# Kernel tuning notes

Hardware: AMD Instinct MI355X
Metric: run time of the kernel (lower is better)

## Reference

```python
import jax, jax.numpy as jnp
import numpy as np

N = 50000        # nodes
E = 1_600_000    # edges (avg degree 32)
G = 512          # graphs in batch
H = 128          # hidden
C_IN = 3
C_MID = 64
C_OUT = 2
EPS = 1e-5


def setup_inputs() -> dict:
    key = jax.random.key(0)
    ks = jax.random.split(key, 16)
    inp = {
        "x": jax.random.normal(ks[0], (N, C_IN), dtype=jnp.float32),
        "edge_index": jax.random.randint(ks[1], (2, E), 0, N, dtype=jnp.int64),
        "batch": jnp.sort(jax.random.randint(ks[2], (N,), 0, G, dtype=jnp.int64)),
        # GCNConv weights (PyG: out = norm_agg(x @ W) + b)
        "W1": jax.random.normal(ks[3], (C_IN, H), dtype=jnp.float32) / np.sqrt(C_IN),
        "b1": jnp.zeros((H,), jnp.float32),
        "W2": jax.random.normal(ks[4], (H, H), dtype=jnp.float32) / np.sqrt(H),
        "b2": jnp.zeros((H,), jnp.float32),
        "W3": jax.random.normal(ks[5], (H, H), dtype=jnp.float32) / np.sqrt(H),
        "b3": jnp.zeros((H,), jnp.float32),
        # BatchNorm affine params (input_bn, bn1, bn2, bn3)
        "bn0_g": jnp.ones((C_IN,), jnp.float32), "bn0_b": jnp.zeros((C_IN,), jnp.float32),
        "bn1_g": jnp.ones((H,), jnp.float32), "bn1_b": jnp.zeros((H,), jnp.float32),
        "bn2_g": jnp.ones((H,), jnp.float32), "bn2_b": jnp.zeros((H,), jnp.float32),
        "bn3_g": jnp.ones((H,), jnp.float32), "bn3_b": jnp.zeros((H,), jnp.float32),
        # classifier MLP
        "Wc1": jax.random.normal(ks[6], (H, C_MID), dtype=jnp.float32) / np.sqrt(H),
        "bc1": jnp.zeros((C_MID,), jnp.float32),
        "Wc2": jax.random.normal(ks[7], (C_MID, C_OUT), dtype=jnp.float32) / np.sqrt(C_MID),
        "bc2": jnp.zeros((C_OUT,), jnp.float32),
    }
    return inp


def _batchnorm(h, g, b):
    # training-mode BN over node dim (biased variance, as torch uses for normalization)
    m = h.mean(axis=0)
    v = jnp.mean((h - m) ** 2, axis=0)
    return (h - m) * jax.lax.rsqrt(v + EPS) * g + b


def _gcn_conv(h, W, b, src, dst, deg_inv_sqrt, deg_inv):
    # PyG GCNConv: symmetric normalization with self-loops.
    hw = h @ W                                        # [N, out]
    coef = deg_inv_sqrt[src] * deg_inv_sqrt[dst]      # [E]
    msg = hw[src] * coef[:, None]                     # [E, out]
    agg = jax.ops.segment_sum(msg, dst, num_segments=N)
    agg = agg + hw * deg_inv[:, None]                 # self-loop term (norm = 1/deg)
    return agg + b


def reference(x, edge_index, batch, W1, b1, W2, b2, W3, b3,
              bn0_g, bn0_b, bn1_g, bn1_b, bn2_g, bn2_b, bn3_g, bn3_b,
              Wc1, bc1, Wc2, bc2):
    src, dst = edge_index[0], edge_index[1]
    # degree with self-loops (in-degree at dst + 1)
    deg = jax.ops.segment_sum(jnp.ones((E,), jnp.float32), dst, num_segments=N) + 1.0
    deg_inv_sqrt = jax.lax.rsqrt(deg)
    deg_inv = 1.0 / deg

    h = _batchnorm(x, bn0_g, bn0_b)
    h = _batchnorm(jax.nn.relu(_gcn_conv(h, W1, b1, src, dst, deg_inv_sqrt, deg_inv)), bn1_g, bn1_b)
    h = _batchnorm(jax.nn.relu(_gcn_conv(h, W2, b2, src, dst, deg_inv_sqrt, deg_inv)), bn2_g, bn2_b)
    h = _batchnorm(jax.nn.relu(_gcn_conv(h, W3, b3, src, dst, deg_inv_sqrt, deg_inv)), bn3_g, bn3_b)

    # global mean pool over graphs
    sums = jax.ops.segment_sum(h, batch, num_segments=G)            # [G, H]
    cnts = jax.ops.segment_sum(jnp.ones((N,), jnp.float32), batch, num_segments=G)
    pooled = sums / jnp.maximum(cnts, 1.0)[:, None]

    # classifier (dropout = identity in eval)
    z = jax.nn.relu(pooled @ Wc1 + bc1)
    return z @ Wc2 + bc2
```

## Files before the change

kernel.cpp:

```cpp
#include <hip/hip_runtime.h>

#define NEPS 1e-5f

__device__ inline unsigned int bfpack(float a, float b) {
  unsigned int ua = __float_as_uint(a), ub = __float_as_uint(b);
  ua += 0x7fff + ((ua >> 16) & 1);
  ub += 0x7fff + ((ub >> 16) & 1);
  return (ua >> 16) | (ub & 0xffff0000u);
}
__device__ inline float bflo(unsigned int u) { return __uint_as_float(u << 16); }
__device__ inline float bfhi(unsigned int u) { return __uint_as_float(u & 0xffff0000u); }

__device__ inline int blockScan256(int v, int t, int* tmp) {
  int lane = t & 63, w = t >> 6;
  #pragma unroll
  for (int off = 1; off < 64; off <<= 1) {
    int u = __shfl_up(v, off);
    if (lane >= off) v += u;
  }
  if (lane == 63) tmp[w] = v;
  __syncthreads();
  int add = 0;
  for (int k = 0; k < w; k++) add += tmp[k];
  return v + add;
}

__global__ __launch_bounds__(256) void k_hist(const int* __restrict__ ei,
                                              int* __restrict__ gh_pad, int E_) {
  __shared__ int h[256];
  int t = threadIdx.x;
  h[t] = 0;
  __syncthreads();
  int i = blockIdx.x * 256 + t;
  int stride = gridDim.x * 256;
  for (int e = i; e < E_; e += stride) atomicAdd(&h[ei[E_ + e] >> 8], 1);
  __syncthreads();
  int c = h[t];
  if (c) atomicAdd(&gh_pad[t * 16], c);
}

__global__ __launch_bounds__(256) void k_scan2(const int* __restrict__ gh_pad,
                                               int* __restrict__ b_base,
                                               int* __restrict__ cur_pad, int E_) {
  __shared__ int tmp[4];
  int t = threadIdx.x;
  int c = gh_pad[t * 16];
  int incl = blockScan256(c, t, tmp);
  int excl = incl - c;
  b_base[t] = excl;
  cur_pad[t * 16] = excl;
  if (t == 255) b_base[256] = incl;
}

__global__ __launch_bounds__(256) void k_part(const int* __restrict__ ei,
                                              int* __restrict__ cur_pad,
                                              unsigned int* __restrict__ kp, int E_) {
  __shared__ int lh[256], lbase[256];
  int t = threadIdx.x;
  int start = blockIdx.x * 8192;
  int end = min(start + 8192, E_);
  lh[t] = 0;
  __syncthreads();
  for (int e = start + t; e < end; e += 256) atomicAdd(&lh[ei[E_ + e] >> 8], 1);
  __syncthreads();
  int c = lh[t];
  if (c) lbase[t] = atomicAdd(&cur_pad[t * 16], c);
  __syncthreads();
  lh[t] = 0;
  __syncthreads();
  for (int e = start + t; e < end; e += 256) {
    int d = ei[E_ + e], s = ei[e];
    int bin = d >> 8;
    int slot = atomicAdd(&lh[bin], 1);
    kp[lbase[bin] + slot] = ((unsigned int)d << 16) | (unsigned int)s;
  }
}

__global__ __launch_bounds__(256) void k_bucket(const unsigned int* __restrict__ kp,
                                                const int* __restrict__ b_base,
                                                unsigned short* __restrict__ csr16,
                                                int* __restrict__ row_ptr, int* __restrict__ cnt,
                                                const float* __restrict__ x,
                                                float* __restrict__ dis, float4* __restrict__ xp,
                                                float* __restrict__ stats, int N_) {
  __shared__ int cur[256], offL[256], tmp[4];
  __shared__ float rs[4][8];
  int t = threadIdx.x, b = blockIdx.x;
  int seg0 = b_base[b], seg1 = b_base[b + 1];
  cur[t] = 0;
  __syncthreads();
  for (int e = seg0 + t; e < seg1; e += 256) atomicAdd(&cur[(kp[e] >> 16) & 255], 1);
  __syncthreads();
  int c = cur[t];
  int incl = blockScan256(c, t, tmp);
  offL[t] = incl - c;
  __syncthreads();
  cur[t] = 0;
  __syncthreads();
  for (int e = seg0 + t; e < seg1; e += 256) {
    unsigned int v = kp[e];
    int dl = (v >> 16) & 255;
    int slot = atomicAdd(&cur[dl], 1);
    csr16[seg0 + offL[dl] + slot] = (unsigned short)(v & 0xffffu);
  }
  int n = b * 256 + t;
  float s1[3] = {0, 0, 0}, s2[3] = {0, 0, 0};
  if (n < N_) {
    row_ptr[n] = seg0 + offL[t];
    cnt[n] = c;
    float dg = (float)c + 1.0f;
    float ds_ = rsqrtf(dg);
    dis[n] = ds_;
    float x0 = x[n * 3 + 0], x1 = x[n * 3 + 1], x2 = x[n * 3 + 2];
    float4 v; v.x = ds_ * x0; v.y = ds_ * x1; v.z = ds_ * x2; v.w = ds_;
    xp[n] = v;
    s1[0] = x0; s1[1] = x1; s1[2] = x2;
    s2[0] = x0 * x0; s2[1] = x1 * x1; s2[2] = x2 * x2;
  }
  #pragma unroll
  for (int cc = 0; cc < 3; cc++) {
    for (int off = 32; off > 0; off >>= 1) {
      s1[cc] += __shfl_down(s1[cc], off);
      s2[cc] += __shfl_down(s2[cc], off);
    }
  }
  int lane = t & 63, w = t >> 6;
  if (lane == 0) {
    rs[w][0] = s1[0]; rs[w][1] = s1[1]; rs[w][2] = s1[2]; rs[w][3] = 0.f;
    rs[w][4] = s2[0]; rs[w][5] = s2[1]; rs[w][6] = s2[2]; rs[w][7] = 0.f;
  }
  __syncthreads();
  if (t < 8 && t != 3 && t != 7) {
    float a = rs[0][t] + rs[1][t] + rs[2][t] + rs[3][t];
    atomicAdd(&stats[t], a);
  }
}

__global__ __launch_bounds__(256) void k_layer1(const float4* __restrict__ xp,
                                                const unsigned short* __restrict__ csr16,
                                                const int* __restrict__ row_ptr,
                                                const int* __restrict__ cnt,
                                                const float* __restrict__ stats,
                                                const float* __restrict__ g0,
                                                const float* __restrict__ b0,
                                                const float* __restrict__ W1,
                                                const float* __restrict__ b1,
                                                unsigned short* __restrict__ yb,
                                                float* __restrict__ Sp,
                                                int N_) {
  __shared__ float wl[5 * 128];
  int t = threadIdx.x;
  float a_[3], dd_[3];
  #pragma unroll
  for (int c = 0; c < 3; c++) {
    float m = stats[c] / N_;
    float v = stats[4 + c] / N_ - m * m;
    float sc = g0[c] * rsqrtf(v + NEPS);
    a_[c] = sc; dd_[c] = b0[c] - m * sc;
  }
  for (int i = t; i < 384; i += 256) wl[i] = a_[i >> 7] * W1[i];
  for (int i = t; i < 128; i += 256) {
    wl[384 + i] = fmaf(dd_[0], W1[i], fmaf(dd_[1], W1[128 + i], dd_[2] * W1[256 + i]));
    wl[512 + i] = b1[i];
  }
  __syncthreads();
  int lane = t & 63, w = t >> 6;
  int c0 = lane * 2;
  float2 w0 = *(const float2*)&wl[c0];
  float2 w1 = *(const float2*)&wl[128 + c0];
  float2 w2 = *(const float2*)&wl[256 + c0];
  float2 uu = *(const float2*)&wl[384 + c0];
  float2 bb = *(const float2*)&wl[512 + c0];
  int wid = blockIdx.x * 4 + w;
  int nw = gridDim.x * 4;
  float s1x = 0, s1y = 0, s2x = 0, s2y = 0;
  for (int n = wid; n < N_; n += nw) {
    int dg = cnt[n];
    int base = row_ptr[n];
    float a0 = 0, a1 = 0, a2 = 0, sd = 0;
    for (int chunk = 0; chunk < dg; chunk += 64) {
      int cc = min(64, dg - chunk);
      if (lane < cc) {
        float4 v = xp[csr16[base + chunk + lane]];
        a0 += v.x; a1 += v.y; a2 += v.z; sd += v.w;
      }
    }
    #pragma unroll
    for (int m = 1; m < 64; m <<= 1) {
      a0 += __shfl_xor(a0, m);
      a1 += __shfl_xor(a1, m);
      a2 += __shfl_xor(a2, m);
      sd += __shfl_xor(sd, m);
    }
    float4 xn = xp[n];
    float dn = xn.w;
    a0 += xn.x; a1 += xn.y; a2 += xn.z; sd += xn.w;
    float z0 = dn * a0, z1 = dn * a1, z2 = dn * a2, zw = dn * sd;
    float ox = fmaxf(fmaf(z0, w0.x, fmaf(z1, w1.x, fmaf(z2, w2.x, fmaf(zw, uu.x, bb.x)))), 0.f);
    float oy = fmaxf(fmaf(z0, w0.y, fmaf(z1, w1.y, fmaf(z2, w2.y, fmaf(zw, uu.y, bb.y)))), 0.f);
    s1x += ox; s1y += oy; s2x += ox * ox; s2y += oy * oy;
    *(unsigned int*)&yb[(size_t)n * 128 + c0] = bfpack(ox, oy);
  }
  __shared__ float rs[4][64][4];
  rs[w][lane][0] = s1x; rs[w][lane][1] = s1y;
  rs[w][lane][2] = s2x; rs[w][lane][3] = s2y;
  __syncthreads();
  int s = t >> 7, c = t & 127;
  int lsrc = c >> 1, sl = (s << 1) | (c & 1);
  float a = rs[0][lsrc][sl] + rs[1][lsrc][sl] + rs[2][lsrc][sl] + rs[3][lsrc][sl];
  float* basep = Sp + (blockIdx.x & 7) * 256;
  atomicAdd(&basep[s * 128 + c], a);
}

__global__ __launch_bounds__(256) void k_gemm(const unsigned short* __restrict__ yb,
                                              const float* __restrict__ W,
                                              const float* __restrict__ Sp,
                                              const float* __restrict__ g_,
                                              const float* __restrict__ b_,
                                              const float* __restrict__ dis,
                                              unsigned short* __restrict__ hwb, int N_) {
  int t = threadIdx.x;
  if (blockIdx.x == 0 && t < 64) ((unsigned int*)&hwb[(size_t)N_ * 128])[t] = 0;
  __shared__ float scs[128], shs[128];
  __shared__ float yl[64][128];
  if (t < 128) {
    float m_s = 0, v_s = 0;
    #pragma unroll
    for (int p = 0; p < 8; p++) { m_s += Sp[p * 256 + t]; v_s += Sp[p * 256 + 128 + t]; }
    float m = m_s / N_;
    float v = v_s / N_ - m * m;
    float s = g_[t] * rsqrtf(v + NEPS);
    scs[t] = s; shs[t] = b_[t] - m * s;
  }
  __syncthreads();
  int base = blockIdx.x * 64;
  for (int i = t; i < 64 * 16; i += 256) {
    int r = i >> 4;
    int q = (i & 15) * 8;
    int n = base + r;
    float o[8];
    if (n < N_) {
      uint4 v = *(const uint4*)&yb[(size_t)n * 128 + q];
      unsigned int uu[4] = {v.x, v.y, v.z, v.w};
      #pragma unroll
      for (int k = 0; k < 4; k++) {
        o[k * 2]     = fmaf(bflo(uu[k]), scs[q + k * 2],     shs[q + k * 2]);
        o[k * 2 + 1] = fmaf(bfhi(uu[k]), scs[q + k * 2 + 1], shs[q + k * 2 + 1]);
      }
    } else {
      #pragma unroll
      for (int k = 0; k < 8; k++) o[k] = 0.f;
    }
    #pragma unroll
    for (int k = 0; k < 8; k++) yl[r][q + k] = o[k];
  }
  __syncthreads();
  int tn = t >> 5, tj = t & 31;
  float4 acc[8];
  #pragma unroll
  for (int r = 0; r < 8; r++) acc[r] = float4{0, 0, 0, 0};
  for (int kk = 0; kk < 128; kk++) {
    float4 wv = *(const float4*)&W[kk * 128 + tj * 4];
    #pragma unroll
    for (int r = 0; r < 8; r++) {
      float yv = yl[tn * 8 + r][kk];
      acc[r].x = fmaf(yv, wv.x, acc[r].x);
      acc[r].y = fmaf(yv, wv.y, acc[r].y);
      acc[r].z = fmaf(yv, wv.z, acc[r].z);
      acc[r].w = fmaf(yv, wv.w, acc[r].w);
    }
  }
  #pragma unroll
  for (int r = 0; r < 8; r++) {
    int n = base + tn * 8 + r;
    if (n < N_) {
      float dn = dis[n];
      uint2 o;
      o.x = bfpack(acc[r].x * dn, acc[r].y * dn);
      o.y = bfpack(acc[r].z * dn, acc[r].w * dn);
      *(uint2*)&hwb[(size_t)n * 128 + tj * 4] = o;
    }
  }
}

template <int FUSE_POOL>
__global__ __launch_bounds__(256) void k_gatherb(const unsigned short* __restrict__ hwb,
                                                 const unsigned short* __restrict__ csr16,
                                                 const int* __restrict__ row_ptr,
                                                 const int* __restrict__ cnt,
                                                 const float* __restrict__ dis,
                                                 const float* __restrict__ bL,
                                                 unsigned short* __restrict__ yb,
                                                 float* __restrict__ Sp,
                                                 const int* __restrict__ batch,
                                                 float* __restrict__ pooled, int N_) {
  int t = threadIdx.x;
  int lane = t & 63, w = t >> 6;
  int g16 = lane >> 4, l16 = lane & 15;
  int c0 = l16 * 8 + g16 * 2;
  float2 bb = *(const float2*)&bL[c0];
  const uint4* hw4 = (const uint4*)hwb;
  int wid = blockIdx.x * 4 + w;
  int nw = gridDim.x * 4;
  float s1a = 0, s1b = 0, s2a = 0, s2b = 0;
  for (int n = wid; n < N_; n += nw) {
    int dg = cnt[n];
    int base = row_ptr[n];
    float acc[8] = {0, 0, 0, 0, 0, 0, 0, 0};
    for (int chunk = 0; chunk < dg; chunk += 64) {
      int cc = min(64, dg - chunk);
      int idx = (lane < cc) ? (int)csr16[base + chunk + lane] : N_;
      int nit = (cc + 3) >> 2;
      #pragma unroll 8
      for (int i = 0; i < nit; i++) {
        int s_ = __shfl(idx, i * 4 + g16);
        uint4 v = hw4[(size_t)s_ * 16 + l16];
        acc[0] += bflo(v.x); acc[1] += bfhi(v.x);
        acc[2] += bflo(v.y); acc[3] += bfhi(v.y);
        acc[4] += bflo(v.z); acc[5] += bfhi(v.z);
        acc[6] += bflo(v.w); acc[7] += bfhi(v.w);
      }
    }
    float dn = dis[n];
    {
      uint4 v = hw4[(size_t)n * 16 + l16];
      float wc = (g16 == 0) ? 1.f : 0.f;
      acc[0] = fmaf(wc, bflo(v.x), acc[0]); acc[1] = fmaf(wc, bfhi(v.x), acc[1]);
      acc[2] = fmaf(wc, bflo(v.y), acc[2]); acc[3] = fmaf(wc, bfhi(v.y), acc[3]);
      acc[4] = fmaf(wc, bflo(v.z), acc[4]); acc[5] = fmaf(wc, bfhi(v.z), acc[5]);
      acc[6] = fmaf(wc, bflo(v.w), acc[6]); acc[7] = fmaf(wc, bfhi(v.w), acc[7]);
    }
    #pragma unroll
    for (int k = 0; k < 8; k++) {
      acc[k] += __shfl_xor(acc[k], 16);
      acc[k] += __shfl_xor(acc[k], 32);
    }
    float ta = (g16 & 1) ? acc[2] : acc[0];
    float tb = (g16 & 1) ? acc[6] : acc[4];
    float va = (g16 & 2) ? tb : ta;
    float tc = (g16 & 1) ? acc[3] : acc[1];
    float td = (g16 & 1) ? acc[7] : acc[5];
    float vb = (g16 & 2) ? td : tc;
    float ox = fmaxf(fmaf(va, dn, bb.x), 0.f);
    float oy = fmaxf(fmaf(vb, dn, bb.y), 0.f);
    s1a += ox; s1b += oy; s2a += ox * ox; s2b += oy * oy;
    if (FUSE_POOL) {
      int g = batch[n];
      atomicAdd(&pooled[g * 128 + c0], ox);
      atomicAdd(&pooled[g * 128 + c0 + 1], oy);
    } else {
      *(unsigned int*)&yb[(size_t)n * 128 + c0] = bfpack(ox, oy);
    }
  }
  __shared__ float rs[4][64][4];
  rs[w][lane][0] = s1a; rs[w][lane][1] = s1b;
  rs[w][lane][2] = s2a; rs[w][lane][3] = s2b;
  __syncthreads();
  int s = t >> 7, c = t & 127;
  int lsrc = (c >> 3) | (((c & 7) >> 1) << 4);
  int sl = (s << 1) | (c & 1);
  float a = rs[0][lsrc][sl] + rs[1][lsrc][sl] + rs[2][lsrc][sl] + rs[3][lsrc][sl];
  float* basep = Sp + (blockIdx.x & 7) * 256;
  atomicAdd(&basep[s * 128 + c], a);
}

__device__ inline int lb_dev(const int* b, int n, int v) {
  int lo = 0, hi = n;
  while (lo < hi) { int mid = (lo + hi) >> 1; if (b[mid] < v) lo = mid + 1; else hi = mid; }
  return lo;
}

__global__ void k_cls(const float* __restrict__ pooled, const int* __restrict__ batch,
                      const float* __restrict__ Sp,
                      const float* __restrict__ g_, const float* __restrict__ b_,
                      const float* __restrict__ Wc1, const float* __restrict__ bc1,
                      const float* __restrict__ Wc2, const float* __restrict__ bc2,
                      float* __restrict__ out, int N_, int G_) {
  __shared__ float p[128];
  __shared__ float z[64];
  __shared__ int s_lo, s_hi;
  int g = blockIdx.x, t = threadIdx.x;
  if (t == 0) s_lo = lb_dev(batch, N_, g);
  if (t == 1) s_hi = lb_dev(batch, N_, g + 1);
  __syncthreads();
  float inv = 1.f / fmaxf((float)(s_hi - s_lo), 1.f);
  for (int k = t; k < 128; k += 64) {
    float m_s = 0, v_s = 0;
    #pragma unroll
    for (int q = 0; q < 8; q++) { m_s += Sp[q * 256 + k]; v_s += Sp[q * 256 + 128 + k]; }
    float m = m_s / N_;
    float v = v_s / N_ - m * m;
    float s = g_[k] * rsqrtf(v + NEPS);
    float sh = b_[k] - m * s;
    p[k] = fmaf(pooled[g * 128 + k] * inv, s, sh);
  }
  __syncthreads();
  float acc = bc1[t];
  for (int k = 0; k < 128; k++) acc = fmaf(p[k], Wc1[k * 64 + t], acc);
  z[t] = fmaxf(acc, 0.f);
  __syncthreads();
  if (t < 2) {
    float o = bc2[t];
    for (int j = 0; j < 64; j++) o = fmaf(z[j], Wc2[j * 2 + t], o);
    out[g * 2 + t] = o;
  }
}

extern "C" void kernel_launch(void* const* d_in, const int* in_sizes, int n_in,
                              void* d_out, int out_size, void* d_ws, size_t ws_size,
                              hipStream_t stream) {
  const float* x    = (const float*)d_in[0];
  const int*   ei   = (const int*)d_in[1];
  const int*   batch= (const int*)d_in[2];
  const float* W1   = (const float*)d_in[3];
  const float* b1   = (const float*)d_in[4];
  const float* W2   = (const float*)d_in[5];
  const float* b2   = (const float*)d_in[6];
  const float* W3   = (const float*)d_in[7];
  const float* b3   = (const float*)d_in[8];
  const float* bn0g = (const float*)d_in[9];
  const float* bn0b = (const float*)d_in[10];
  const float* bn1g = (const float*)d_in[11];
  const float* bn1b = (const float*)d_in[12];
  const float* bn2g = (const float*)d_in[13];
  const float* bn2b = (const float*)d_in[14];
  const float* bn3g = (const float*)d_in[15];
  const float* bn3b = (const float*)d_in[16];
  const float* Wc1  = (const float*)d_in[17];
  const float* bc1  = (const float*)d_in[18];
  const float* Wc2  = (const float*)d_in[19];
  const float* bc2  = (const float*)d_in[20];

  const int N_ = in_sizes[2];
  const int E_ = in_sizes[1] / 2;
  const int G_ = out_size / 2;
  const int NB = (N_ + 255) / 256;

  char* ws = (char*)d_ws;
  size_t off = 0;
  auto A = [&](size_t bytes) { size_t o = off; off = (off + bytes + 255) & ~(size_t)255; return o; };
  size_t o_gh    = A(256 * 16 * 4);
  size_t o_stats = A((size_t)(256 + 3 * 2048) * 4);
  size_t o_pool  = A((size_t)G_ * 128 * 4);
  size_t zero_end = off;
  size_t o_cur   = A(256 * 16 * 4);
  size_t o_bbase = A(257 * 4);
  size_t o_kp    = A((size_t)E_ * 4);
  size_t o_csr16 = A(((size_t)E_ + 64) * 2);
  size_t o_rowp  = A((size_t)N_ * 4);
  size_t o_cnt   = A((size_t)N_ * 4);
  size_t o_dis   = A((size_t)N_ * 4);
  size_t o_xp    = A((size_t)N_ * 16);
  size_t o_ybA   = A((size_t)N_ * 128 * 2);
  size_t o_ybB   = A((size_t)N_ * 128 * 2);
  size_t o_bufAh = A(((size_t)N_ + 1) * 128 * 2);
  (void)ws_size; (void)n_in;

  int*   gh_pad  = (int*)(ws + o_gh);
  float* stats   = (float*)(ws + o_stats);
  float* Sp1     = stats + 256;
  float* Sp2     = stats + 256 + 2048;
  float* Sp3     = stats + 256 + 4096;
  float* pooled  = (float*)(ws + o_pool);
  int*   cur_pad = (int*)(ws + o_cur);
  int*   b_base  = (int*)(ws + o_bbase);
  unsigned int* kp = (unsigned int*)(ws + o_kp);
  unsigned short* csr16 = (unsigned short*)(ws + o_csr16);
  int*   row_ptr = (int*)(ws + o_rowp);
  int*   cnt     = (int*)(ws + o_cnt);
  float* dis     = (float*)(ws + o_dis);
  float4* xp     = (float4*)(ws + o_xp);
  unsigned short* ybA = (unsigned short*)(ws + o_ybA);
  unsigned short* ybB = (unsigned short*)(ws + o_ybB);
  unsigned short* bufAh = (unsigned short*)(ws + o_bufAh);

  hipMemsetAsync(ws, 0, zero_end, stream);

  k_hist<<<256, 256, 0, stream>>>(ei, gh_pad, E_);
  k_scan2<<<1, 256, 0, stream>>>(gh_pad, b_base, cur_pad, E_);
  k_part<<<(E_ + 8191) / 8192, 256, 0, stream>>>(ei, cur_pad, kp, E_);
  k_bucket<<<NB, 256, 0, stream>>>(kp, b_base, csr16, row_ptr, cnt, x, dis, xp, stats, N_);

  k_layer1<<<2048, 256, 0, stream>>>(xp, csr16, row_ptr, cnt, stats, bn0g, bn0b, W1, b1,
                                     ybA, Sp1, N_);

  k_gemm<<<(N_ + 63) / 64, 256, 0, stream>>>(ybA, W2, Sp1, bn1g, bn1b, dis, bufAh, N_);
  k_gatherb<0><<<2048, 256, 0, stream>>>(bufAh, csr16, row_ptr, cnt, dis, b2, ybB, Sp2,
                                         batch, pooled, N_);

  k_gemm<<<(N_ + 63) / 64, 256, 0, stream>>>(ybB, W3, Sp2, bn2g, bn2b, dis, bufAh, N_);
  k_gatherb<1><<<2048, 256, 0, stream>>>(bufAh, csr16, row_ptr, cnt, dis, b3, nullptr, Sp3,
                                         batch, pooled, N_);

  k_cls<<<G_, 64, 0, stream>>>(pooled, batch, Sp3, bn3g, bn3b, Wc1, bc1, Wc2, bc2,
                               (float*)d_out, N_, G_);
}
```

Measured before the change: 293.1 us.

## Split hidden features into four 32-channel column slabs for cache-friendly gather

```diff
diff --git a/kernel.cpp b/kernel.cpp
--- a/kernel.cpp
+++ b/kernel.cpp
@@ -218,9 +218,12 @@
                                               const float* __restrict__ g_,
                                               const float* __restrict__ b_,
                                               const float* __restrict__ dis,
-                                              unsigned short* __restrict__ hwb, int N_) {
-  int t = threadIdx.x;
-  if (blockIdx.x == 0 && t < 64) ((unsigned int*)&hwb[(size_t)N_ * 128])[t] = 0;
+                                              unsigned short* __restrict__ hwc, int N_) {
+  int t = threadIdx.x;
+  if (blockIdx.x == 0 && t < 64) {
+    int c = t >> 4, p = t & 15;
+    ((unsigned int*)(hwc + ((size_t)c * (N_ + 1) + N_) * 32))[p] = 0;
+  }
   __shared__ float scs[128], shs[128];
   __shared__ float yl[64][128];
   if (t < 128) {
@@ -278,13 +281,14 @@
       uint2 o;
       o.x = bfpack(acc[r].x * dn, acc[r].y * dn);
       o.y = bfpack(acc[r].z * dn, acc[r].w * dn);
-      *(uint2*)&hwb[(size_t)n * 128 + tj * 4] = o;
+      size_t ro = ((size_t)(tj >> 3) * (N_ + 1) + n) * 32 + (tj & 7) * 4;
+      *(uint2*)&hwc[ro] = o;
     }
   }
 }
 
 template <int FUSE_POOL>
-__global__ __launch_bounds__(256) void k_gatherb(const unsigned short* __restrict__ hwb,
+__global__ __launch_bounds__(256) void k_gatherc(const unsigned short* __restrict__ hwc,
                                                  const unsigned short* __restrict__ csr16,
                                                  const int* __restrict__ row_ptr,
                                                  const int* __restrict__ cnt,
@@ -297,71 +301,65 @@
   int t = threadIdx.x;
   int lane = t & 63, w = t >> 6;
   int g16 = lane >> 4, l16 = lane & 15;
-  int c0 = l16 * 8 + g16 * 2;
-  float2 bb = *(const float2*)&bL[c0];
-  const uint4* hw4 = (const uint4*)hwb;
-  int wid = blockIdx.x * 4 + w;
-  int nw = gridDim.x * 4;
+  int chunk = blockIdx.x >> 11;
+  int bid = blockIdx.x & 2047;
+  int cbase = chunk * 32;
+  int ca = cbase + l16 * 2;
+  float2 bb = *(const float2*)&bL[ca];
+  const unsigned int* hw32 = (const unsigned int*)(hwc + (size_t)chunk * (N_ + 1) * 32);
+  int wid = bid * 4 + w;
+  int nw = 2048 * 4;
   float s1a = 0, s1b = 0, s2a = 0, s2b = 0;
   for (int n = wid; n < N_; n += nw) {
     int dg = cnt[n];
     int base = row_ptr[n];
-    float acc[8] = {0, 0, 0, 0, 0, 0, 0, 0};
-    for (int chunk = 0; chunk < dg; chunk += 64) {
-      int cc = min(64, dg - chunk);
-      int idx = (lane < cc) ? (int)csr16[base + chunk + lane] : N_;
+    float a0 = 0, a1 = 0;
+    for (int ch = 0; ch < dg; ch += 64) {
+      int cc = min(64, dg - ch);
+      int idx = (lane < cc) ? (int)csr16[base + ch + lane] : N_;
       int nit = (cc + 3) >> 2;
       #pragma unroll 8
       for (int i = 0; i < nit; i++) {
         int s_ = __shfl(idx, i * 4 + g16);
-        uint4 v = hw4[(size_t)s_ * 16 + l16];
-        acc[0] += bflo(v.x); acc[1] += bfhi(v.x);
-        acc[2] += bflo(v.y); acc[3] += bfhi(v.y);
-        acc[4] += bflo(v.z); acc[5] += bfhi(v.z);
-        acc[6] += bflo(v.w); acc[7] += bfhi(v.w);
+        unsigned int v = hw32[s_ * 16 + l16];
+        a0 += bflo(v); a1 += bfhi(v);
       }
     }
     float dn = dis[n];
     {
-      uint4 v = hw4[(size_t)n * 16 + l16];
+      unsigned int v = hw32[n * 16 + l16];
       float wc = (g16 == 0) ? 1.f : 0.f;
-      acc[0] = fmaf(wc, bflo(v.x), acc[0]); acc[1] = fmaf(wc, bfhi(v.x), acc[1]);
-      acc[2] = fmaf(wc, bflo(v.y), acc[2]); acc[3] = fmaf(wc, bfhi(v.y), acc[3]);
-      acc[4] = fmaf(wc, bflo(v.z), acc[4]); acc[5] = fmaf(wc, bfhi(v.z), acc[5]);
-      acc[6] = fmaf(wc, bflo(v.w), acc[6]); acc[7] = fmaf(wc, bfhi(v.w), acc[7]);
-    }
-    #pragma unroll
-    for (int k = 0; k < 8; k++) {
-      acc[k] += __shfl_xor(acc[k], 16);
-      acc[k] += __shfl_xor(acc[k], 32);
-    }
-    float ta = (g16 & 1) ? acc[2] : acc[0];
-    float tb = (g16 & 1) ? acc[6] : acc[4];
-    float va = (g16 & 2) ? tb : ta;
-    float tc = (g16 & 1) ? acc[3] : acc[1];
-    float td = (g16 & 1) ? acc[7] : acc[5];
-    float vb = (g16 & 2) ? td : tc;
-    float ox = fmaxf(fmaf(va, dn, bb.x), 0.f);
-    float oy = fmaxf(fmaf(vb, dn, bb.y), 0.f);
-    s1a += ox; s1b += oy; s2a += ox * ox; s2b += oy * oy;
-    if (FUSE_POOL) {
-      int g = batch[n];
-      atomicAdd(&pooled[g * 128 + c0], ox);
-      atomicAdd(&pooled[g * 128 + c0 + 1], oy);
-    } else {
-      *(unsigned int*)&yb[(size_t)n * 128 + c0] = bfpack(ox, oy);
-    }
-  }
-  __shared__ float rs[4][64][4];
-  rs[w][lane][0] = s1a; rs[w][lane][1] = s1b;
-  rs[w][lane][2] = s2a; rs[w][lane][3] = s2b;
-  __syncthreads();
-  int s = t >> 7, c = t & 127;
-  int lsrc = (c >> 3) | (((c & 7) >> 1) << 4);
-  int sl = (s << 1) | (c & 1);
-  float a = rs[0][lsrc][sl] + rs[1][lsrc][sl] + rs[2][lsrc][sl] + rs[3][lsrc][sl];
-  float* basep = Sp + (blockIdx.x & 7) * 256;
-  atomicAdd(&basep[s * 128 + c], a);
+      a0 = fmaf(wc, bflo(v), a0);
+      a1 = fmaf(wc, bfhi(v), a1);
+    }
+    a0 += __shfl_xor(a0, 16); a0 += __shfl_xor(a0, 32);
+    a1 += __shfl_xor(a1, 16); a1 += __shfl_xor(a1, 32);
+    float ox = fmaxf(fmaf(a0, dn, bb.x), 0.f);
+    float oy = fmaxf(fmaf(a1, dn, bb.y), 0.f);
+    if (g16 == 0) {
+      s1a += ox; s1b += oy; s2a += ox * ox; s2b += oy * oy;
+      if (FUSE_POOL) {
+        int g = batch[n];
+        atomicAdd(&pooled[g * 128 + ca], ox);
+        atomicAdd(&pooled[g * 128 + ca + 1], oy);
+      } else {
+        *(unsigned int*)&yb[(size_t)n * 128 + ca] = bfpack(ox, oy);
+      }
+    }
+  }
+  __shared__ float rs[4][16][4];
+  if (g16 == 0) {
+    rs[w][l16][0] = s1a; rs[w][l16][1] = s1b;
+    rs[w][l16][2] = s2a; rs[w][l16][3] = s2b;
+  }
+  __syncthreads();
+  if (t < 64) {
+    int l = t >> 2, j = t & 3;
+    float a = rs[0][l][j] + rs[1][l][j] + rs[2][l][j] + rs[3][l][j];
+    int channel = cbase + l * 2 + (j & 1);
+    int kind = j >> 1;
+    atomicAdd(&Sp[(bid & 7) * 256 + kind * 128 + channel], a);
+  }
 }
 
 __device__ inline int lb_dev(const int* b, int n, int v) {
@@ -453,7 +451,7 @@
   size_t o_xp    = A((size_t)N_ * 16);
   size_t o_ybA   = A((size_t)N_ * 128 * 2);
   size_t o_ybB   = A((size_t)N_ * 128 * 2);
-  size_t o_bufAh = A(((size_t)N_ + 1) * 128 * 2);
+  size_t o_hwc   = A((size_t)4 * (N_ + 1) * 32 * 2);
   (void)ws_size; (void)n_in;
 
   int*   gh_pad  = (int*)(ws + o_gh);
@@ -472,7 +470,7 @@
   float4* xp     = (float4*)(ws + o_xp);
   unsigned short* ybA = (unsigned short*)(ws + o_ybA);
   unsigned short* ybB = (unsigned short*)(ws + o_ybB);
-  unsigned short* bufAh = (unsigned short*)(ws + o_bufAh);
+  unsigned short* hwc = (unsigned short*)(ws + o_hwc);
 
   hipMemsetAsync(ws, 0, zero_end, stream);
 
@@ -484,13 +482,13 @@
   k_layer1<<<2048, 256, 0, stream>>>(xp, csr16, row_ptr, cnt, stats, bn0g, bn0b, W1, b1,
                                      ybA, Sp1, N_);
 
-  k_gemm<<<(N_ + 63) / 64, 256, 0, stream>>>(ybA, W2, Sp1, bn1g, bn1b, dis, bufAh, N_);
-  k_gatherb<0><<<2048, 256, 0, stream>>>(bufAh, csr16, row_ptr, cnt, dis, b2, ybB, Sp2,
-                                         batch, pooled, N_);
-
-  k_gemm<<<(N_ + 63) / 64, 256, 0, stream>>>(ybB, W3, Sp2, bn2g, bn2b, dis, bufAh, N_);
-  k_gatherb<1><<<2048, 256, 0, stream>>>(bufAh, csr16, row_ptr, cnt, dis, b3, nullptr, Sp3,
-                                         batch, pooled, N_);
+  k_gemm<<<(N_ + 63) / 64, 256, 0, stream>>>(ybA, W2, Sp1, bn1g, bn1b, dis, hwc, N_);
+  k_gatherc<0><<<4 * 2048, 256, 0, stream>>>(hwc, csr16, row_ptr, cnt, dis, b2, ybB, Sp2,
+                                             batch, pooled, N_);
+
+  k_gemm<<<(N_ + 63) / 64, 256, 0, stream>>>(ybB, W3, Sp2, bn2g, bn2b, dis, hwc, N_);
+  k_gatherc<1><<<4 * 2048, 256, 0, stream>>>(hwc, csr16, row_ptr, cnt, dis, b3, nullptr, Sp3,
+                                             batch, pooled, N_);
 
   k_cls<<<G_, 64, 0, stream>>>(pooled, batch, Sp3, bn3g, bn3b, Wc1, bc1, Wc2, bc2,
                                (float*)d_out, N_, G_);
```

New measurement: 421.7 us. 1.44x slower.
